# Performance work log

Hardware: AMD Instinct MI355X
Metric: run time of the kernel (lower is better)

The kernel has to match this reference:

```python
import jax, jax.numpy as jnp
import numpy as np

V, E, B, T = 128, 8, 64, 512
HID = (512, 512, 512)


def setup_inputs() -> dict:
    key = jax.random.key(0)
    ks = jax.random.split(key, 16)
    inp = {"tokens": jax.random.randint(ks[0], (B, T), 0, V, dtype=jnp.int32)}
    inp["emb"] = jax.random.normal(ks[1], (V, E), dtype=jnp.float32) * 0.05
    d_in = E
    ki = 2
    for l, u in enumerate(HID):
        inp[f"W{l}"] = jax.random.normal(ks[ki], (d_in, 4 * u), dtype=jnp.float32) / np.float32(np.sqrt(d_in)); ki += 1
        inp[f"U{l}"] = jax.random.normal(ks[ki], (u, 4 * u), dtype=jnp.float32) / np.float32(np.sqrt(u)); ki += 1
        # Keras unit_forget_bias=True: forget-gate bias initialized to 1
        inp[f"b{l}"] = jnp.zeros((4 * u,), jnp.float32).at[u:2 * u].set(1.0)
        d_in = u
    inp["Wd"] = jax.random.normal(ks[ki], (HID[-1], V), dtype=jnp.float32) / np.float32(np.sqrt(HID[-1]))
    inp["bd"] = jnp.zeros((V,), jnp.float32)
    return inp


def _lstm(x, W, U, b):
    # x: [B,T,D]; Keras gate order i,f,g,o; sigmoid recurrent activation, tanh activation.
    bsz = x.shape[0]
    u = U.shape[0]
    xw = jnp.einsum('btd,dg->btg', x, W) + b  # precompute input projections [B,T,4u]

    def step(carry, z_t):
        h, c = carry
        z = z_t + h @ U
        i, f, g, o = jnp.split(z, 4, axis=-1)
        i = jax.nn.sigmoid(i)
        f = jax.nn.sigmoid(f)
        g = jnp.tanh(g)
        o = jax.nn.sigmoid(o)
        c = f * c + i * g
        h = o * jnp.tanh(c)
        return (h, c), h

    init = (jnp.zeros((bsz, u), x.dtype), jnp.zeros((bsz, u), x.dtype))
    _, hs = jax.lax.scan(step, init, jnp.swapaxes(xw, 0, 1))  # time-major scan
    return jnp.swapaxes(hs, 0, 1)  # [B,T,u]


def reference(tokens, emb, W0, U0, b0, W1, U1, b1, W2, U2, b2, Wd, bd):
    x = emb[tokens]  # [B,T,E]
    for W, U, b in ((W0, U0, b0), (W1, U1, b1), (W2, U2, b2)):
        x = _lstm(x, W, U, b)
    logits = jnp.einsum('btu,uv->btv', x, Wd) + bd
    return jax.nn.softmax(logits, axis=-1)
```

## Files before the change

kernel.cpp:

```cpp
#include <hip/hip_runtime.h>
#include <cstdint>
#include <cstddef>

#define TT 512
#define DZP 65

#define O_BAR   0
#define O_HT    1024
#define WS_ZERO (O_HT + 6*32768)
#define O_CWP0  WS_ZERO
#define O_CWP1  (O_CWP0 + 256*512*8)
#define O_CWP2  (O_CWP1 + 256*1024*8)
#define O_W0P   (O_CWP2 + 256*1024*8)
#define WS_ALL  (O_W0P + 256*64)

#define BARR(g) (64 + (g) * 16)
#define BGRP    32
#define BREL(g) (512 + (g) * 16)

typedef float f4v __attribute__((ext_vector_type(4)));

__device__ __forceinline__ void coh_ld16(f4v* dst, const f4v* addr) {
  asm volatile("global_load_dwordx4 %0, %1, off sc0 sc1" : "=v"(*dst) : "v"(addr));
}
__device__ __forceinline__ void coh_st4(float* addr, float v) {
  asm volatile("global_store_dword %0, %1, off sc0 sc1" :: "v"(addr), "v"(v) : "memory");
}
__device__ __forceinline__ void vm_wait0() {
  asm volatile("s_waitcnt vmcnt(0)" ::: "memory");
  __builtin_amdgcn_sched_barrier(0);
}

__device__ __forceinline__ void grid_barrier(unsigned* bar, unsigned target, int tid, int bid) {
  __syncthreads();
  if (tid == 0) {
    asm volatile("s_waitcnt vmcnt(0)" ::: "memory");
    const unsigned g = (unsigned)bid & 15u;
    const unsigned o = atomicAdd(&bar[BARR(g)], 1u);
    if ((o & 15u) == 15u) {
      const unsigned o2 = atomicAdd(&bar[BGRP], 1u);
      if ((o2 & 15u) == 15u) {
#pragma unroll
        for (int q = 0; q < 16; ++q) atomicExch(&bar[BREL(q)], target);
      }
    }
    unsigned spins = 0;
    while (atomicAdd(&bar[BREL(g)], 0u) != target) {
      if (++spins > 30000u) break;
      __builtin_amdgcn_s_sleep(2);
    }
  }
  __syncthreads();
}

__device__ __forceinline__ void lstm_phase(
    int l0flag, int Ktot, const float* wsec,
    const float* belowT, const float* ownT,
    const float* __restrict__ bias, float* hdstT, float* creg,
    const int* __restrict__ tokens, const float* __restrict__ emb,
    const float* w0l, int t,
    double* dz, int p, int tid)
{
  const int lane = tid & 63;
  const int w = __builtin_amdgcn_readfirstlane(tid >> 6);
  const int Kq = Ktot >> 3;
  const int k0 = w * Kq;
  const float* hsrc = (Ktot == 512 || w < 4) ? belowT : ownT;
  const int kbase = (Ktot == 512 || w < 4) ? k0 : k0 - 512;
  const f4v* hq = (const f4v*)hsrc;
  const int nch = Kq >> 6;
  double d[8] = {0.0, 0.0, 0.0, 0.0, 0.0, 0.0, 0.0, 0.0};

  for (int ch = 0; ch < nch; ++ch) {
    const int kq0 = (kbase >> 2) + ch * 16;
    f4v h[16];
#pragma unroll
    for (int i = 0; i < 16; ++i)
      coh_ld16(&h[i], hq + (size_t)(kq0 + i) * 64 + lane);
    vm_wait0();
#pragma unroll
    for (int g2 = 0; g2 < 2; ++g2) {
      float s8[8] = {0.f, 0.f, 0.f, 0.f, 0.f, 0.f, 0.f, 0.f};
#pragma unroll
      for (int i = 0; i < 8; ++i) {
        const f4v hv = h[g2 * 8 + i];
#pragma unroll
        for (int q = 0; q < 4; ++q) {
          const float xk = hv[q];
          const int kl = k0 + ch * 64 + g2 * 32 + i * 4 + q;
          const float4 wa = *(const float4*)&wsec[(size_t)kl * 8];
          const float4 wb = *(const float4*)&wsec[(size_t)kl * 8 + 4];
          s8[0] = fmaf(xk, wa.x, s8[0]); s8[1] = fmaf(xk, wa.y, s8[1]);
          s8[2] = fmaf(xk, wa.z, s8[2]); s8[3] = fmaf(xk, wa.w, s8[3]);
          s8[4] = fmaf(xk, wb.x, s8[4]); s8[5] = fmaf(xk, wb.y, s8[5]);
          s8[6] = fmaf(xk, wb.z, s8[6]); s8[7] = fmaf(xk, wb.w, s8[7]);
        }
      }
#pragma unroll
      for (int j = 0; j < 8; ++j) d[j] += (double)s8[j];
    }
  }

  if (l0flag && w == 0) {
    const int tok = tokens[lane * TT + t];
    float s8[8] = {0.f, 0.f, 0.f, 0.f, 0.f, 0.f, 0.f, 0.f};
#pragma unroll
    for (int e = 0; e < 8; ++e) {
      const float xe = emb[tok * 8 + e];
      const float4 wa = *(const float4*)&w0l[e * 8];
      const float4 wb = *(const float4*)&w0l[e * 8 + 4];
      s8[0] = fmaf(xe, wa.x, s8[0]); s8[1] = fmaf(xe, wa.y, s8[1]);
      s8[2] = fmaf(xe, wa.z, s8[2]); s8[3] = fmaf(xe, wa.w, s8[3]);
      s8[4] = fmaf(xe, wb.x, s8[4]); s8[5] = fmaf(xe, wb.y, s8[5]);
      s8[6] = fmaf(xe, wb.z, s8[6]); s8[7] = fmaf(xe, wb.w, s8[7]);
    }
#pragma unroll
    for (int j = 0; j < 8; ++j) d[j] += (double)s8[j];
  }

#pragma unroll
  for (int j = 0; j < 8; ++j) dz[(j * 8 + w) * DZP + lane] = d[j];
  __syncthreads();

  if (tid < 128) {
    const int m = tid & 63, uu = tid >> 6;
    const int u = 2 * p + uu;
    float zf[4];
#pragma unroll
    for (int g = 0; g < 4; ++g) {
      double zs = (double)bias[(g << 9) + u];
#pragma unroll
      for (int w8 = 0; w8 < 8; ++w8)
        zs += dz[((g * 2 + uu) * 8 + w8) * DZP + m];
      zf[g] = (float)zs;
    }
    const float iv = 1.f / (1.f + expf(-zf[0]));
    const float fv = 1.f / (1.f + expf(-zf[1]));
    const float gv = tanhf(zf[2]);
    const float ov = 1.f / (1.f + expf(-zf[3]));
    const float cn = fv * (*creg) + iv * gv;
    *creg = cn;
    coh_st4(&hdstT[((u >> 2) * 64 + m) * 4 + (u & 3)], ov * tanhf(cn));
  }
  __syncthreads();
}

__global__ void __launch_bounds__(256)
rnn_prep(float* __restrict__ ws,
         const float* __restrict__ W0, const float* __restrict__ U0,
         const float* __restrict__ W1, const float* __restrict__ U1,
         const float* __restrict__ W2, const float* __restrict__ U2)
{
  const int tid = (int)threadIdx.x;
  const int bid = (int)blockIdx.x;
  const int gtid = bid * 256 + tid;
  for (int i = gtid; i < WS_ZERO; i += 768 * 256) ws[i] = 0.f;

  float* CWP0 = ws + O_CWP0;
  float* CWP1 = ws + O_CWP1;
  float* CWP2 = ws + O_CWP2;
  float* W0P  = ws + O_W0P;
  if (bid < 256) {
    const int p = bid;
    for (int k = tid; k < 512; k += 256)
#pragma unroll
      for (int j = 0; j < 8; ++j) {
        const int col = ((j >> 1) << 9) + 2 * p + (j & 1);
        CWP0[((size_t)p * 512 + k) * 8 + j] = U0[(size_t)k * 2048 + col];
      }
    if (tid < 64) {
      const int e = tid >> 3, j = tid & 7;
      const int col = ((j >> 1) << 9) + 2 * p + (j & 1);
      W0P[p * 64 + e * 8 + j] = W0[(size_t)e * 2048 + col];
    }
  } else if (bid < 512) {
    const int p = bid - 256;
    for (int k = tid; k < 1024; k += 256) {
      const float* src = (k < 512) ? &W1[(size_t)k * 2048] : &U1[(size_t)(k - 512) * 2048];
#pragma unroll
      for (int j = 0; j < 8; ++j) {
        const int col = ((j >> 1) << 9) + 2 * p + (j & 1);
        CWP1[((size_t)p * 1024 + k) * 8 + j] = src[col];
      }
    }
  } else {
    const int p = bid - 512;
    for (int k = tid; k < 1024; k += 256) {
      const float* src = (k < 512) ? &W2[(size_t)k * 2048] : &U2[(size_t)(k - 512) * 2048];
#pragma unroll
      for (int j = 0; j < 8; ++j) {
        const int col = ((j >> 1) << 9) + 2 * p + (j & 1);
        CWP2[((size_t)p * 1024 + k) * 8 + j] = src[col];
      }
    }
  }
}

__global__ void __launch_bounds__(512, 1)
rnn_all(const int* __restrict__ tokens, const float* __restrict__ emb,
        const float* __restrict__ b0, const float* __restrict__ b1,
        const float* __restrict__ b2,
        const float* __restrict__ Wd, const float* __restrict__ bd,
        float* __restrict__ out, float* __restrict__ ws)
{
  __shared__ __align__(16) float wl[20544];
  __shared__ double dz[64 * DZP];
  __shared__ float red[512];
  const int tid = (int)threadIdx.x;
  const int p = (int)blockIdx.x;
  unsigned* bar = (unsigned*)ws;
  float* ht = ws + O_HT;

  {
    const float* s0 = ws + O_CWP0 + (size_t)p * 4096;
    for (int i = tid; i < 4096; i += 512) wl[i] = s0[i];
    const float* s1 = ws + O_CWP1 + (size_t)p * 8192;
    for (int i = tid; i < 8192; i += 512) wl[4096 + i] = s1[i];
    const float* s2 = ws + O_CWP2 + (size_t)p * 8192;
    for (int i = tid; i < 8192; i += 512) wl[12288 + i] = s2[i];
    if (tid < 64) wl[20480 + tid] = ws[O_W0P + p * 64 + tid];
  }
  float c0 = 0.f, c1 = 0.f, c2 = 0.f;
  __syncthreads();

  for (int s = 0; s < 515; ++s) {
    const int po = (s + 1) & 1;
    const int pw = s & 1;
    float* h0po = ht + (size_t)(0 * 2 + po) * 32768;
    float* h1po = ht + (size_t)(1 * 2 + po) * 32768;
    float* h2po = ht + (size_t)(2 * 2 + po) * 32768;
    float* h0pw = ht + (size_t)(0 * 2 + pw) * 32768;
    float* h1pw = ht + (size_t)(1 * 2 + pw) * 32768;
    float* h2pw = ht + (size_t)(2 * 2 + pw) * 32768;

    if (s < 512)
      lstm_phase(1, 512, wl, h0po, h0po, b0, h0pw, &c0, tokens, emb,
                 wl + 20480, s, dz, p, tid);
    if (s >= 1 && s < 513)
      lstm_phase(0, 1024, wl + 4096, h0po, h1po, b1, h1pw, &c1,
                 nullptr, nullptr, nullptr, 0, dz, p, tid);
    if (s >= 2 && s < 514)
      lstm_phase(0, 1024, wl + 12288, h1po, h2po, b2, h2pw, &c2,
                 nullptr, nullptr, nullptr, 0, dz, p, tid);

    if (s >= 3 && p < 64) {
      const int r = p;
      const f4v* h2q = (const f4v*)h2po;
      const int col = tid & 127, kq4 = tid >> 7;
      double acc = 0.0;
      for (int ch = 0; ch < 4; ++ch) {
        f4v h[8];
#pragma unroll
        for (int i = 0; i < 8; ++i)
          coh_ld16(&h[i], h2q + (size_t)(kq4 * 32 + ch * 8 + i) * 64 + r);
        vm_wait0();
        float sa = 0.f;
#pragma unroll
        for (int i = 0; i < 8; ++i)
#pragma unroll
          for (int q = 0; q < 4; ++q) {
            const int k = (kq4 * 32 + ch * 8 + i) * 4 + q;
            sa = fmaf(h[i][q], Wd[(size_t)k * 128 + col], sa);
          }
        acc += (double)sa;
      }
      dz[tid] = acc;
      __syncthreads();
      float xlg = -3.0e38f;
      if (tid < 128)
        xlg = (float)(dz[tid] + dz[tid + 128] + dz[tid + 256] + dz[tid + 384]
                      + (double)bd[col]);
      red[tid] = xlg;                       __syncthreads();
      if (tid < 256) red[tid] = fmaxf(red[tid], red[tid + 256]); __syncthreads();
      if (tid < 128) red[tid] = fmaxf(red[tid], red[tid + 128]); __syncthreads();
      if (tid < 64)  red[tid] = fmaxf(red[tid], red[tid + 64]);  __syncthreads();
      if (tid < 32)  red[tid] = fmaxf(red[tid], red[tid + 32]);  __syncthreads();
      if (tid < 16)  red[tid] = fmaxf(red[tid], red[tid + 16]);  __syncthreads();
      if (tid < 8)   red[tid] = fmaxf(red[tid], red[tid + 8]);   __syncthreads();
      if (tid < 4)   red[tid] = fmaxf(red[tid], red[tid + 4]);   __syncthreads();
      if (tid < 2)   red[tid] = fmaxf(red[tid], red[tid + 2]);   __syncthreads();
      if (tid < 1)   red[tid] = fmaxf(red[tid], red[tid + 1]);   __syncthreads();
      const float mx = red[0];              __syncthreads();
      const float ex = (tid < 128) ? expf(xlg - mx) : 0.f;
      red[tid] = ex;                        __syncthreads();
      if (tid < 256) red[tid] += red[tid + 256]; __syncthreads();
      if (tid < 128) red[tid] += red[tid + 128]; __syncthreads();
      if (tid < 64)  red[tid] += red[tid + 64];  __syncthreads();
      if (tid < 32)  red[tid] += red[tid + 32];  __syncthreads();
      if (tid < 16)  red[tid] += red[tid + 16];  __syncthreads();
      if (tid < 8)   red[tid] += red[tid + 8];   __syncthreads();
      if (tid < 4)   red[tid] += red[tid + 4];   __syncthreads();
      if (tid < 2)   red[tid] += red[tid + 2];   __syncthreads();
      if (tid < 1)   red[tid] += red[tid + 1];   __syncthreads();
      const float inv = 1.f / red[0];
      if (tid < 128) out[((size_t)r * 512 + (s - 3)) * 128 + tid] = ex * inv;
    }

    grid_barrier(bar, (unsigned)(s + 1), tid, p);
  }
}

extern "C" void kernel_launch(void* const* d_in, const int* in_sizes, int n_in,
                              void* d_out, int out_size, void* d_ws, size_t ws_size,
                              hipStream_t stream) {
  (void)in_sizes; (void)n_in; (void)out_size;
  if (ws_size < (size_t)WS_ALL * 4) return;
  const int*   tokens = (const int*)d_in[0];
  const float* emb = (const float*)d_in[1];
  const float* W0 = (const float*)d_in[2];
  const float* U0 = (const float*)d_in[3];
  const float* b0 = (const float*)d_in[4];
  const float* W1 = (const float*)d_in[5];
  const float* U1 = (const float*)d_in[6];
  const float* b1 = (const float*)d_in[7];
  const float* W2 = (const float*)d_in[8];
  const float* U2 = (const float*)d_in[9];
  const float* b2 = (const float*)d_in[10];
  const float* Wd = (const float*)d_in[11];
  const float* bd = (const float*)d_in[12];
  float* out = (float*)d_out;
  float* ws  = (float*)d_ws;

  hipLaunchKernelGGL(rnn_prep, dim3(768), dim3(256), 0, stream,
                     ws, W0, U0, W1, U1, W2, U2);
  hipLaunchKernelGGL(rnn_all, dim3(256), dim3(512), 0, stream,
                     tokens, emb, b0, b1, b2, Wd, bd, out, ws);
}
```

Before: 14.76 ms.

## Software-pipeline hidden-state loads across the three LSTM layers per step

Replaces the per-layer lstm_phase calls with an inlined, software-pipelined schedule. Global loads of the next layer's hidden-state chunks are issued while the current chunk is being computed, using rotating register buffers and partial vmcnt waits. The gate epilogue is spread across all 8 waves at 16 lanes each, biases are preloaded into registers, and the dense-head h2 loads are all issued before a single wait. It also raises the launch-bounds occupancy hint to 2, which limits registers even though the large shared memory footprint may still allow only one block per CU. The added register pressure could cause spills.

```diff
diff --git a/kernel.cpp b/kernel.cpp
--- a/kernel.cpp
+++ b/kernel.cpp
@@ -26,9 +26,60 @@
 __device__ __forceinline__ void coh_st4(float* addr, float v) {
   asm volatile("global_store_dword %0, %1, off sc0 sc1" :: "v"(addr), "v"(v) : "memory");
 }
-__device__ __forceinline__ void vm_wait0() {
-  asm volatile("s_waitcnt vmcnt(0)" ::: "memory");
-  __builtin_amdgcn_sched_barrier(0);
+#define VMWAIT(n) do { asm volatile("s_waitcnt vmcnt(" #n ")" ::: "memory"); \
+                       __builtin_amdgcn_sched_barrier(0); } while (0)
+#define LGKMBAR() do { asm volatile("s_waitcnt lgkmcnt(0)\n\ts_barrier" ::: "memory"); } while (0)
+
+__device__ __forceinline__ void issue8(f4v h[8], const f4v* hq, int kq0, int lane) {
+  const f4v* base = hq + (size_t)kq0 * 64 + lane;
+#pragma unroll
+  for (int i = 0; i < 8; ++i) coh_ld16(&h[i], base + i * 64);
+}
+
+__device__ __forceinline__ void comp8(const f4v h[8], const float* wk, double d[8]) {
+  float s8[8] = {0.f, 0.f, 0.f, 0.f, 0.f, 0.f, 0.f, 0.f};
+#pragma unroll
+  for (int i = 0; i < 8; ++i) {
+#pragma unroll
+    for (int q = 0; q < 4; ++q) {
+      const float xk = h[i][q];
+      const float4 wa = *(const float4*)&wk[(i * 4 + q) * 8];
+      const float4 wb = *(const float4*)&wk[(i * 4 + q) * 8 + 4];
+      s8[0] = fmaf(xk, wa.x, s8[0]); s8[1] = fmaf(xk, wa.y, s8[1]);
+      s8[2] = fmaf(xk, wa.z, s8[2]); s8[3] = fmaf(xk, wa.w, s8[3]);
+      s8[4] = fmaf(xk, wb.x, s8[4]); s8[5] = fmaf(xk, wb.y, s8[5]);
+      s8[6] = fmaf(xk, wb.z, s8[6]); s8[7] = fmaf(xk, wb.w, s8[7]);
+    }
+  }
+#pragma unroll
+  for (int j = 0; j < 8; ++j) d[j] += (double)s8[j];
+}
+
+__device__ __forceinline__ void epilogue(
+    double* dz, const float br[4], float* creg, float* hdstT,
+    int p, int w, int lane)
+{
+  if (lane < 16) {
+    const int uu = w >> 2;
+    const int em = (w & 3) * 16 + lane;
+    float zf[4];
+#pragma unroll
+    for (int g = 0; g < 4; ++g) {
+      double zs = (double)br[g];
+#pragma unroll
+      for (int w8 = 0; w8 < 8; ++w8)
+        zs += dz[((g * 2 + uu) * 8 + w8) * DZP + em];
+      zf[g] = (float)zs;
+    }
+    const float iv = 1.f / (1.f + expf(-zf[0]));
+    const float fv = 1.f / (1.f + expf(-zf[1]));
+    const float gv = tanhf(zf[2]);
+    const float ov = 1.f / (1.f + expf(-zf[3]));
+    const float cn = fv * (*creg) + iv * gv;
+    *creg = cn;
+    const int u = 2 * p + uu;
+    coh_st4(&hdstT[((u >> 2) * 64 + em) * 4 + (u & 3)], ov * tanhf(cn));
+  }
 }
 
 __device__ __forceinline__ void grid_barrier(unsigned* bar, unsigned target, int tid, int bid) {
@@ -49,98 +100,6 @@
       if (++spins > 30000u) break;
       __builtin_amdgcn_s_sleep(2);
     }
-  }
-  __syncthreads();
-}
-
-__device__ __forceinline__ void lstm_phase(
-    int l0flag, int Ktot, const float* wsec,
-    const float* belowT, const float* ownT,
-    const float* __restrict__ bias, float* hdstT, float* creg,
-    const int* __restrict__ tokens, const float* __restrict__ emb,
-    const float* w0l, int t,
-    double* dz, int p, int tid)
-{
-  const int lane = tid & 63;
-  const int w = __builtin_amdgcn_readfirstlane(tid >> 6);
-  const int Kq = Ktot >> 3;
-  const int k0 = w * Kq;
-  const float* hsrc = (Ktot == 512 || w < 4) ? belowT : ownT;
-  const int kbase = (Ktot == 512 || w < 4) ? k0 : k0 - 512;
-  const f4v* hq = (const f4v*)hsrc;
-  const int nch = Kq >> 6;
-  double d[8] = {0.0, 0.0, 0.0, 0.0, 0.0, 0.0, 0.0, 0.0};
-
-  for (int ch = 0; ch < nch; ++ch) {
-    const int kq0 = (kbase >> 2) + ch * 16;
-    f4v h[16];
-#pragma unroll
-    for (int i = 0; i < 16; ++i)
-      coh_ld16(&h[i], hq + (size_t)(kq0 + i) * 64 + lane);
-    vm_wait0();
-#pragma unroll
-    for (int g2 = 0; g2 < 2; ++g2) {
-      float s8[8] = {0.f, 0.f, 0.f, 0.f, 0.f, 0.f, 0.f, 0.f};
-#pragma unroll
-      for (int i = 0; i < 8; ++i) {
-        const f4v hv = h[g2 * 8 + i];
-#pragma unroll
-        for (int q = 0; q < 4; ++q) {
-          const float xk = hv[q];
-          const int kl = k0 + ch * 64 + g2 * 32 + i * 4 + q;
-          const float4 wa = *(const float4*)&wsec[(size_t)kl * 8];
-          const float4 wb = *(const float4*)&wsec[(size_t)kl * 8 + 4];
-          s8[0] = fmaf(xk, wa.x, s8[0]); s8[1] = fmaf(xk, wa.y, s8[1]);
-          s8[2] = fmaf(xk, wa.z, s8[2]); s8[3] = fmaf(xk, wa.w, s8[3]);
-          s8[4] = fmaf(xk, wb.x, s8[4]); s8[5] = fmaf(xk, wb.y, s8[5]);
-          s8[6] = fmaf(xk, wb.z, s8[6]); s8[7] = fmaf(xk, wb.w, s8[7]);
-        }
-      }
-#pragma unroll
-      for (int j = 0; j < 8; ++j) d[j] += (double)s8[j];
-    }
-  }
-
-  if (l0flag && w == 0) {
-    const int tok = tokens[lane * TT + t];
-    float s8[8] = {0.f, 0.f, 0.f, 0.f, 0.f, 0.f, 0.f, 0.f};
-#pragma unroll
-    for (int e = 0; e < 8; ++e) {
-      const float xe = emb[tok * 8 + e];
-      const float4 wa = *(const float4*)&w0l[e * 8];
-      const float4 wb = *(const float4*)&w0l[e * 8 + 4];
-      s8[0] = fmaf(xe, wa.x, s8[0]); s8[1] = fmaf(xe, wa.y, s8[1]);
-      s8[2] = fmaf(xe, wa.z, s8[2]); s8[3] = fmaf(xe, wa.w, s8[3]);
-      s8[4] = fmaf(xe, wb.x, s8[4]); s8[5] = fmaf(xe, wb.y, s8[5]);
-      s8[6] = fmaf(xe, wb.z, s8[6]); s8[7] = fmaf(xe, wb.w, s8[7]);
-    }
-#pragma unroll
-    for (int j = 0; j < 8; ++j) d[j] += (double)s8[j];
-  }
-
-#pragma unroll
-  for (int j = 0; j < 8; ++j) dz[(j * 8 + w) * DZP + lane] = d[j];
-  __syncthreads();
-
-  if (tid < 128) {
-    const int m = tid & 63, uu = tid >> 6;
-    const int u = 2 * p + uu;
-    float zf[4];
-#pragma unroll
-    for (int g = 0; g < 4; ++g) {
-      double zs = (double)bias[(g << 9) + u];
-#pragma unroll
-      for (int w8 = 0; w8 < 8; ++w8)
-        zs += dz[((g * 2 + uu) * 8 + w8) * DZP + m];
-      zf[g] = (float)zs;
-    }
-    const float iv = 1.f / (1.f + expf(-zf[0]));
-    const float fv = 1.f / (1.f + expf(-zf[1]));
-    const float gv = tanhf(zf[2]);
-    const float ov = 1.f / (1.f + expf(-zf[3]));
-    const float cn = fv * (*creg) + iv * gv;
-    *creg = cn;
-    coh_st4(&hdstT[((u >> 2) * 64 + m) * 4 + (u & 3)], ov * tanhf(cn));
   }
   __syncthreads();
 }
@@ -196,7 +155,7 @@
   }
 }
 
-__global__ void __launch_bounds__(512, 1)
+__global__ void __launch_bounds__(512, 2)
 rnn_all(const int* __restrict__ tokens, const float* __restrict__ emb,
         const float* __restrict__ b0, const float* __restrict__ b1,
         const float* __restrict__ b2,
@@ -208,6 +167,8 @@
   __shared__ float red[512];
   const int tid = (int)threadIdx.x;
   const int p = (int)blockIdx.x;
+  const int lane = tid & 63;
+  const int w = __builtin_amdgcn_readfirstlane(tid >> 6);
   unsigned* bar = (unsigned*)ws;
   float* ht = ws + O_HT;
 
@@ -219,6 +180,15 @@
     const float* s2 = ws + O_CWP2 + (size_t)p * 8192;
     for (int i = tid; i < 8192; i += 512) wl[12288 + i] = s2[i];
     if (tid < 64) wl[20480 + tid] = ws[O_W0P + p * 64 + tid];
+  }
+  float br0[4], br1[4], br2[4];
+  {
+    const int uu = w >> 2;
+#pragma unroll
+    for (int g = 0; g < 4; ++g) {
+      const int c_ = (g << 9) + 2 * p + uu;
+      br0[g] = b0[c_]; br1[g] = b1[c_]; br2[g] = b2[c_];
+    }
   }
   float c0 = 0.f, c1 = 0.f, c2 = 0.f;
   __syncthreads();
@@ -233,34 +203,118 @@
     float* h1pw = ht + (size_t)(1 * 2 + pw) * 32768;
     float* h2pw = ht + (size_t)(2 * 2 + pw) * 32768;
 
-    if (s < 512)
-      lstm_phase(1, 512, wl, h0po, h0po, b0, h0pw, &c0, tokens, emb,
-                 wl + 20480, s, dz, p, tid);
-    if (s >= 1 && s < 513)
-      lstm_phase(0, 1024, wl + 4096, h0po, h1po, b1, h1pw, &c1,
-                 nullptr, nullptr, nullptr, 0, dz, p, tid);
-    if (s >= 2 && s < 514)
-      lstm_phase(0, 1024, wl + 12288, h1po, h2po, b2, h2pw, &c2,
-                 nullptr, nullptr, nullptr, 0, dz, p, tid);
+    const f4v* hqL0 = (const f4v*)h0po;  const int kqA = w * 16;
+    const f4v* hqL1 = (w < 4) ? (const f4v*)h0po : (const f4v*)h1po;
+    const f4v* hqL2 = (w < 4) ? (const f4v*)h1po : (const f4v*)h2po;
+    const int kqC = (w & 3) * 32;
+    const float* wkL0 = wl + (size_t)(w * 64) * 8;
+    const float* wkL1 = wl + 4096 + (size_t)(w * 128) * 8;
+    const float* wkL2 = wl + 12288 + (size_t)(w * 128) * 8;
+
+    double d[8] = {0, 0, 0, 0, 0, 0, 0, 0};
+    if (s < 512 && w == 0) {
+      const int tok = tokens[lane * TT + s];
+      const float4 e0 = *(const float4*)&emb[tok * 8];
+      const float4 e1 = *(const float4*)&emb[tok * 8 + 4];
+      float s8[8] = {0.f, 0.f, 0.f, 0.f, 0.f, 0.f, 0.f, 0.f};
+#pragma unroll
+      for (int e = 0; e < 8; ++e) {
+        const float xe = (e < 4) ? ((const float*)&e0)[e] : ((const float*)&e1)[e - 4];
+        const float4 wa = *(const float4*)&wl[20480 + e * 8];
+        const float4 wb = *(const float4*)&wl[20480 + e * 8 + 4];
+        s8[0] = fmaf(xe, wa.x, s8[0]); s8[1] = fmaf(xe, wa.y, s8[1]);
+        s8[2] = fmaf(xe, wa.z, s8[2]); s8[3] = fmaf(xe, wa.w, s8[3]);
+        s8[4] = fmaf(xe, wb.x, s8[4]); s8[5] = fmaf(xe, wb.y, s8[5]);
+        s8[6] = fmaf(xe, wb.z, s8[6]); s8[7] = fmaf(xe, wb.w, s8[7]);
+      }
+#pragma unroll
+      for (int j = 0; j < 8; ++j) d[j] += (double)s8[j];
+    }
+
+    f4v bA[8], bB[8], bC[8];
+
+#define DZFLUSH() do { _Pragma("unroll") \
+    for (int j = 0; j < 8; ++j) { dz[(j * 8 + w) * DZP + lane] = d[j]; d[j] = 0.0; } } while (0)
+
+    if (s >= 2 && s < 512) {
+      issue8(bA, hqL0, kqA, lane);
+      issue8(bB, hqL0, kqA + 8, lane);
+      issue8(bC, hqL1, kqC, lane);
+      VMWAIT(16); comp8(bA, wkL0, d);
+      issue8(bA, hqL1, kqC + 8, lane);
+      VMWAIT(16); comp8(bB, wkL0 + 256, d);
+      DZFLUSH(); LGKMBAR();
+      epilogue(dz, br0, &c0, h0pw, p, w, lane); LGKMBAR();
+      issue8(bB, hqL1, kqC + 16, lane);
+      VMWAIT(17); comp8(bC, wkL1, d);
+      issue8(bC, hqL1, kqC + 24, lane);
+      VMWAIT(17); comp8(bA, wkL1 + 256, d);
+      issue8(bA, hqL2, kqC, lane);
+      VMWAIT(16); comp8(bB, wkL1 + 512, d);
+      issue8(bB, hqL2, kqC + 8, lane);
+      VMWAIT(16); comp8(bC, wkL1 + 768, d);
+      DZFLUSH(); LGKMBAR();
+      epilogue(dz, br1, &c1, h1pw, p, w, lane); LGKMBAR();
+      issue8(bC, hqL2, kqC + 16, lane);
+      VMWAIT(17); comp8(bA, wkL2, d);
+      issue8(bA, hqL2, kqC + 24, lane);
+      VMWAIT(17); comp8(bB, wkL2 + 256, d);
+      VMWAIT(8);  comp8(bC, wkL2 + 512, d);
+      VMWAIT(0);  comp8(bA, wkL2 + 768, d);
+      DZFLUSH(); LGKMBAR();
+      epilogue(dz, br2, &c2, h2pw, p, w, lane); LGKMBAR();
+    } else {
+      if (s < 512) {
+        issue8(bA, hqL0, kqA, lane); issue8(bB, hqL0, kqA + 8, lane);
+        VMWAIT(0); comp8(bA, wkL0, d); comp8(bB, wkL0 + 256, d);
+        DZFLUSH(); LGKMBAR();
+        epilogue(dz, br0, &c0, h0pw, p, w, lane); LGKMBAR();
+      }
+      if (s >= 1 && s < 513) {
+        issue8(bA, hqL1, kqC, lane);      issue8(bB, hqL1, kqC + 8, lane);
+        VMWAIT(8); comp8(bA, wkL1, d);
+        issue8(bC, hqL1, kqC + 16, lane); VMWAIT(8); comp8(bB, wkL1 + 256, d);
+        issue8(bA, hqL1, kqC + 24, lane); VMWAIT(8); comp8(bC, wkL1 + 512, d);
+        VMWAIT(0); comp8(bA, wkL1 + 768, d);
+        DZFLUSH(); LGKMBAR();
+        epilogue(dz, br1, &c1, h1pw, p, w, lane); LGKMBAR();
+      }
+      if (s >= 2 && s < 514) {
+        issue8(bA, hqL2, kqC, lane);      issue8(bB, hqL2, kqC + 8, lane);
+        VMWAIT(8); comp8(bA, wkL2, d);
+        issue8(bC, hqL2, kqC + 16, lane); VMWAIT(8); comp8(bB, wkL2 + 256, d);
+        issue8(bA, hqL2, kqC + 24, lane); VMWAIT(8); comp8(bC, wkL2 + 512, d);
+        VMWAIT(0); comp8(bA, wkL2 + 768, d);
+        DZFLUSH(); LGKMBAR();
+        epilogue(dz, br2, &c2, h2pw, p, w, lane); LGKMBAR();
+      }
+    }
 
     if (s >= 3 && p < 64) {
       const int r = p;
       const f4v* h2q = (const f4v*)h2po;
       const int col = tid & 127, kq4 = tid >> 7;
+      f4v fa[8], fb[8], fc[8], fd[8];
+#pragma unroll
+      for (int i = 0; i < 8; ++i) coh_ld16(&fa[i], h2q + (size_t)(kq4 * 32 + i) * 64 + r);
+#pragma unroll
+      for (int i = 0; i < 8; ++i) coh_ld16(&fb[i], h2q + (size_t)(kq4 * 32 + 8 + i) * 64 + r);
+#pragma unroll
+      for (int i = 0; i < 8; ++i) coh_ld16(&fc[i], h2q + (size_t)(kq4 * 32 + 16 + i) * 64 + r);
+#pragma unroll
+      for (int i = 0; i < 8; ++i) coh_ld16(&fd[i], h2q + (size_t)(kq4 * 32 + 24 + i) * 64 + r);
+      VMWAIT(0);
       double acc = 0.0;
+#pragma unroll
       for (int ch = 0; ch < 4; ++ch) {
-        f4v h[8];
-#pragma unroll
-        for (int i = 0; i < 8; ++i)
-          coh_ld16(&h[i], h2q + (size_t)(kq4 * 32 + ch * 8 + i) * 64 + r);
-        vm_wait0();
+        const f4v* f_ = (ch == 0) ? fa : (ch == 1) ? fb : (ch == 2) ? fc : fd;
         float sa = 0.f;
 #pragma unroll
         for (int i = 0; i < 8; ++i)
 #pragma unroll
           for (int q = 0; q < 4; ++q) {
             const int k = (kq4 * 32 + ch * 8 + i) * 4 + q;
-            sa = fmaf(h[i][q], Wd[(size_t)k * 128 + col], sa);
+            sa = fmaf(f_[i][q], Wd[(size_t)k * 128 + col], sa);
           }
         acc += (double)sa;
       }
```

Result: slower. 29.05 ms (+96.9%).

## Use cached loads for hidden state with acquire fence after grid barrier

Applied to the files above, without the earlier changes.

Hidden-state loads no longer carry the sc0 sc1 bits, so they can hit in cache instead of going coherent to memory. An agent-scope acquire fence after the grid barrier keeps them correct by invalidating stale lines. The vmcnt wait now runs in every thread before the barrier rather than only thread 0. Bias values are also preloaded into registers once, removing per-step global bias reads. The risk is that the fence cost or a coherence subtlety offsets the benefit of cached reads.

```diff
diff --git a/kernel.cpp b/kernel.cpp
--- a/kernel.cpp
+++ b/kernel.cpp
@@ -20,21 +20,19 @@
 
 typedef float f4v __attribute__((ext_vector_type(4)));
 
-__device__ __forceinline__ void coh_ld16(f4v* dst, const f4v* addr) {
-  asm volatile("global_load_dwordx4 %0, %1, off sc0 sc1" : "=v"(*dst) : "v"(addr));
+__device__ __forceinline__ void ld16(f4v* dst, const f4v* addr) {
+  asm volatile("global_load_dwordx4 %0, %1, off" : "=v"(*dst) : "v"(addr));
 }
 __device__ __forceinline__ void coh_st4(float* addr, float v) {
   asm volatile("global_store_dword %0, %1, off sc0 sc1" :: "v"(addr), "v"(v) : "memory");
 }
-__device__ __forceinline__ void vm_wait0() {
+#define VMWAIT(n) do { asm volatile("s_waitcnt vmcnt(" #n ")" ::: "memory"); \
+                       __builtin_amdgcn_sched_barrier(0); } while (0)
+
+__device__ __forceinline__ void grid_barrier(unsigned* bar, unsigned target, int tid, int bid) {
   asm volatile("s_waitcnt vmcnt(0)" ::: "memory");
-  __builtin_amdgcn_sched_barrier(0);
-}
-
-__device__ __forceinline__ void grid_barrier(unsigned* bar, unsigned target, int tid, int bid) {
   __syncthreads();
   if (tid == 0) {
-    asm volatile("s_waitcnt vmcnt(0)" ::: "memory");
     const unsigned g = (unsigned)bid & 15u;
     const unsigned o = atomicAdd(&bar[BARR(g)], 1u);
     if ((o & 15u) == 15u) {
@@ -51,12 +49,13 @@
     }
   }
   __syncthreads();
+  __builtin_amdgcn_fence(__ATOMIC_ACQUIRE, "agent");
 }
 
 __device__ __forceinline__ void lstm_phase(
     int l0flag, int Ktot, const float* wsec,
     const float* belowT, const float* ownT,
-    const float* __restrict__ bias, float* hdstT, float* creg,
+    const float br[4], float* hdstT, float* creg,
     const int* __restrict__ tokens, const float* __restrict__ emb,
     const float* w0l, int t,
     double* dz, int p, int tid)
@@ -76,8 +75,8 @@
     f4v h[16];
 #pragma unroll
     for (int i = 0; i < 16; ++i)
-      coh_ld16(&h[i], hq + (size_t)(kq0 + i) * 64 + lane);
-    vm_wait0();
+      ld16(&h[i], hq + (size_t)(kq0 + i) * 64 + lane);
+    VMWAIT(0);
 #pragma unroll
     for (int g2 = 0; g2 < 2; ++g2) {
       float s8[8] = {0.f, 0.f, 0.f, 0.f, 0.f, 0.f, 0.f, 0.f};
@@ -124,11 +123,10 @@
 
   if (tid < 128) {
     const int m = tid & 63, uu = tid >> 6;
-    const int u = 2 * p + uu;
     float zf[4];
 #pragma unroll
     for (int g = 0; g < 4; ++g) {
-      double zs = (double)bias[(g << 9) + u];
+      double zs = (double)br[g];
 #pragma unroll
       for (int w8 = 0; w8 < 8; ++w8)
         zs += dz[((g * 2 + uu) * 8 + w8) * DZP + m];
@@ -140,6 +138,7 @@
     const float ov = 1.f / (1.f + expf(-zf[3]));
     const float cn = fv * (*creg) + iv * gv;
     *creg = cn;
+    const int u = 2 * p + uu;
     coh_st4(&hdstT[((u >> 2) * 64 + m) * 4 + (u & 3)], ov * tanhf(cn));
   }
   __syncthreads();
@@ -220,6 +219,16 @@
     for (int i = tid; i < 8192; i += 512) wl[12288 + i] = s2[i];
     if (tid < 64) wl[20480 + tid] = ws[O_W0P + p * 64 + tid];
   }
+  float br0[4], br1[4], br2[4], bdr;
+  {
+    const int uu = (tid >> 6) & 1;
+#pragma unroll
+    for (int g = 0; g < 4; ++g) {
+      const int c_ = (g << 9) + 2 * p + uu;
+      br0[g] = b0[c_]; br1[g] = b1[c_]; br2[g] = b2[c_];
+    }
+    bdr = bd[tid & 127];
+  }
   float c0 = 0.f, c1 = 0.f, c2 = 0.f;
   __syncthreads();
 
@@ -234,13 +243,13 @@
     float* h2pw = ht + (size_t)(2 * 2 + pw) * 32768;
 
     if (s < 512)
-      lstm_phase(1, 512, wl, h0po, h0po, b0, h0pw, &c0, tokens, emb,
+      lstm_phase(1, 512, wl, h0po, h0po, br0, h0pw, &c0, tokens, emb,
                  wl + 20480, s, dz, p, tid);
     if (s >= 1 && s < 513)
-      lstm_phase(0, 1024, wl + 4096, h0po, h1po, b1, h1pw, &c1,
+      lstm_phase(0, 1024, wl + 4096, h0po, h1po, br1, h1pw, &c1,
                  nullptr, nullptr, nullptr, 0, dz, p, tid);
     if (s >= 2 && s < 514)
-      lstm_phase(0, 1024, wl + 12288, h1po, h2po, b2, h2pw, &c2,
+      lstm_phase(0, 1024, wl + 12288, h1po, h2po, br2, h2pw, &c2,
                  nullptr, nullptr, nullptr, 0, dz, p, tid);
 
     if (s >= 3 && p < 64) {
@@ -252,8 +261,8 @@
         f4v h[8];
 #pragma unroll
         for (int i = 0; i < 8; ++i)
-          coh_ld16(&h[i], h2q + (size_t)(kq4 * 32 + ch * 8 + i) * 64 + r);
-        vm_wait0();
+          ld16(&h[i], h2q + (size_t)(kq4 * 32 + ch * 8 + i) * 64 + r);
+        VMWAIT(0);
         float sa = 0.f;
 #pragma unroll
         for (int i = 0; i < 8; ++i)
@@ -269,7 +278,7 @@
       float xlg = -3.0e38f;
       if (tid < 128)
         xlg = (float)(dz[tid] + dz[tid + 128] + dz[tid + 256] + dz[tid + 384]
-                      + (double)bd[col]);
+                      + (double)bdr);
       red[tid] = xlg;                       __syncthreads();
       if (tid < 256) red[tid] = fmaxf(red[tid], red[tid + 256]); __syncthreads();
       if (tid < 128) red[tid] = fmaxf(red[tid], red[tid + 128]); __syncthreads();
```

Measured after the change: 21.98 ms. 1.49x slower.
